# Kernel tuning notes

Measured on AMD Instinct MI355X. Metric: run time of the kernel, lower is better.

## Reference

```python
import jax, jax.numpy as jnp
import numpy as np

DIM = 256
HID = DIM * 16

def setup_inputs() -> dict:
    key = jax.random.key(0)
    ks = jax.random.split(key, 6)
    B, L = 4, 2048
    x = jax.random.normal(ks[0], (B, L, DIM), dtype=jnp.float32)
    # nn.Linear(dim, hidden): weight [H, D], bias [H]
    WB = jax.random.normal(ks[1], (HID, DIM), dtype=jnp.float32) / np.sqrt(DIM)
    bB = jax.random.normal(ks[2], (HID,), dtype=jnp.float32) * 0.01
    # nn.Linear(hidden, dim): weight [D, H], bias [D]
    WC = jax.random.normal(ks[3], (DIM, HID), dtype=jnp.float32) / np.sqrt(HID)
    bC = jax.random.normal(ks[4], (DIM,), dtype=jnp.float32) * 0.01
    A = jax.random.normal(ks[5], (HID,), dtype=jnp.float32)
    return {"x": x, "WB": WB, "bB": bB, "WC": WC, "bC": bC, "A": A}

def reference(x, WB, bB, WC, bC, A):
    # b = B(x): [B, L, H]
    b = jnp.einsum('bld,hd->blh', x, WB) + bB
    a = jax.nn.sigmoid(A)  # [H], time-invariant decay
    # h_t = a * h_{t-1} + b_t  (h_0 from zero state) -> associative scan over L
    a_seq = jnp.broadcast_to(a, b.shape)
    def comb(c1, c2):
        a1, u1 = c1
        a2, u2 = c2
        return (a1 * a2, a2 * u1 + u2)
    _, h = jax.lax.associative_scan(comb, (a_seq, b), axis=1)  # [B, L, H]
    # C(h): [B, L, D]
    return jnp.einsum('blh,dh->bld', h, WC) + bC
```

## Files before the change

kernel.cpp:

```cpp
#include <hip/hip_runtime.h>
#include <hip/hip_bf16.h>

#define DIMSZ 256
#define HID 4096
#define BATCH 4
#define SEQ 2048
#define NCH 64
#define CLEN 32
#define SPLITK2 4
#define KCHUNK (HID / SPLITK2)
#define BM2 64

typedef __bf16 bf16_t;
typedef __bf16 bf16x8 __attribute__((ext_vector_type(8)));
typedef float  f32x4  __attribute__((ext_vector_type(4)));

__device__ __forceinline__ float sigmoidf_dev(float x) {
    return 1.0f / (1.0f + __expf(-x));
}

__device__ __forceinline__ void load_lds16(const bf16_t* g, bf16_t* l) {
    __builtin_amdgcn_global_load_lds(
        (const __attribute__((address_space(1))) void*)g,
        (__attribute__((address_space(3))) void*)l,
        16, 0, 0);
}

__device__ __forceinline__ bf16x8 cvt8(const float* p) {
    bf16x8 o;
    #pragma unroll
    for (int j = 0; j < 8; j++) o[j] = (bf16_t)p[j];
    return o;
}

__global__ void prep_kernel(const float* __restrict__ x,
                            const float* __restrict__ WB,
                            const float* __restrict__ WC,
                            bf16_t* __restrict__ xt,
                            bf16_t* __restrict__ WBt,
                            bf16_t* __restrict__ Wt) {
    int i = blockIdx.x * blockDim.x + threadIdx.x;
    if (i < 262144) {
        int lane = i & 63, m16 = (i >> 6) & 511, ks = i >> 15;
        int row = m16 * 16 + (lane & 15);
        int k   = ks * 32 + (lane >> 4) * 8;
        *(bf16x8*)&xt[(size_t)i * 8] = cvt8(&x[(size_t)row * DIMSZ + k]);
    } else if (i < 393216) {
        int j = i - 262144;
        int lane = j & 63, n16 = (j >> 6) & 255, ks = j >> 14;
        int row = n16 * 16 + (lane & 15);
        int k   = ks * 32 + (lane >> 4) * 8;
        *(bf16x8*)&WBt[(size_t)j * 8] = cvt8(&WB[(size_t)row * DIMSZ + k]);
    } else {
        int j = i - 393216;
        int lane = j & 63, g = (j >> 6) & 15, ks = j >> 10;
        int row = g * 16 + (lane & 15);
        int k   = ks * 32 + (lane >> 4) * 8;
        *(bf16x8*)&Wt[(size_t)j * 8] = cvt8(&WC[(size_t)row * HID + k]);
    }
}

__global__ __launch_bounds__(256)
void gemm1_fused(const bf16_t* __restrict__ xt, const bf16_t* __restrict__ WBt,
                 const float* __restrict__ bias, const float* __restrict__ Adecay,
                 bf16_t* __restrict__ Cg, float* __restrict__ totals)
{
    constexpr int N = HID;
    constexpr int LDTILE = 136;
    __shared__ bf16_t tile[128 * LDTILE];

    const int tid = threadIdx.x, wave = tid >> 6, lane = tid & 63;
    const int wm = wave >> 1, wn = wave & 1, q = lane >> 4, r16 = lane & 15;
    const int mBase = blockIdx.x * 128, nBase = blockIdx.y * 128;
    const int m16Base = blockIdx.x * 8 + wm * 4;
    const int n16Base = blockIdx.y * 8 + wn * 4;

    f32x4 acc[4][4] = {};

    #pragma unroll 2
    for (int ks = 0; ks < 8; ks++) {
        bf16x8 af[4], bfr[4];
        #pragma unroll
        for (int mt = 0; mt < 4; mt++)
            af[mt] = *(const bf16x8*)&xt[(((size_t)ks * 512 + m16Base + mt) * 64 + lane) * 8];
        #pragma unroll
        for (int nt = 0; nt < 4; nt++)
            bfr[nt] = *(const bf16x8*)&WBt[(((size_t)ks * 256 + n16Base + nt) * 64 + lane) * 8];
        #pragma unroll
        for (int mt = 0; mt < 4; mt++)
            #pragma unroll
            for (int nt = 0; nt < 4; nt++)
                acc[mt][nt] = __builtin_amdgcn_mfma_f32_16x16x32_bf16(
                    af[mt], bfr[nt], acc[mt][nt], 0, 0, 0);
    }

    #pragma unroll
    for (int nt = 0; nt < 4; nt++) {
        const int chl = wn * 64 + nt * 16 + r16;
        const float bv = bias[nBase + chl];
        #pragma unroll
        for (int mt = 0; mt < 4; mt++) {
            const int t0 = wm * 64 + mt * 16 + q * 4;
            #pragma unroll
            for (int rg = 0; rg < 4; rg++)
                tile[(t0 + rg) * LDTILE + chl] = (bf16_t)(acc[mt][nt][rg] + bv);
        }
    }
    __syncthreads();

    #pragma unroll
    for (int p = 0; p < 8; p++) {
        const int t = p * 16 + (tid >> 4);
        const int ch8 = (tid & 15) << 3;
        *(bf16x8*)&Cg[(size_t)(mBase + t) * N + nBase + ch8] =
            *(const bf16x8*)&tile[t * LDTILE + ch8];
    }

    #pragma unroll
    for (int t = 0; t < 2; t++) {
        int task = tid + t * 256;
        int ch = task & 127, ck = task >> 7;
        float a = sigmoidf_dev(Adecay[nBase + ch]);
        float tot = 0.f;
        #pragma unroll 8
        for (int i = 0; i < CLEN; i++)
            tot = a * tot + (float)tile[(ck * CLEN + i) * LDTILE + ch];
        int batch = mBase >> 11;
        int cg = ((mBase & 2047) >> 5) + ck;
        totals[(size_t)(batch * NCH + cg) * HID + nBase + ch] = tot;
    }
}

__global__ void scan_carries_kernel(const float* __restrict__ totals,
                                    const float* __restrict__ Adecay,
                                    float* __restrict__ carries)
{
    int gid = blockIdx.x * 64 + threadIdx.x;
    int ch    = gid & (HID - 1);
    int batch = gid >> 12;
    float a = sigmoidf_dev(Adecay[ch]);
    float aC = a;
    #pragma unroll
    for (int i = 0; i < 5; i++) aC *= aC;
    float carry = 0.f;
    #pragma unroll 8
    for (int c = 0; c < NCH; c++) {
        size_t idx = (size_t)(batch * NCH + c) * HID + ch;
        carries[idx] = carry;
        carry = aC * carry + totals[idx];
    }
}

__global__ __launch_bounds__(256)
void gemm2_fused(const bf16_t* __restrict__ bv, const bf16_t* __restrict__ Wt,
                 const float* __restrict__ Adecay, const float* __restrict__ carries,
                 const float* __restrict__ totals, float* __restrict__ P)
{
    constexpr int N = DIMSZ;
    constexpr int CKSTRIDE = BM2 * 32 + 32;
    __shared__ bf16_t hs[8 * CKSTRIDE];

    const int tid = threadIdx.x, wave = tid >> 6, lane = tid & 63;
    const int q = lane >> 4, r16 = lane & 15;
    const int mBase = blockIdx.x * BM2;
    const int kBase = blockIdx.y * KCHUNK;
    const int batch = mBase >> 11;
    const int chunk0 = (mBase & 2047) >> 5;

    f32x4 acc[4][4] = {};

    for (int s = 0; s < KCHUNK / 256; s++) {
        const int chSlab = kBase + s * 256;

        if (s > 0) __syncthreads();

        #pragma unroll
        for (int i = 0; i < 8; i++) {
            int ck = wave * 2 + (i >> 2);
            int g  = i & 3;
            load_lds16(&bv[(size_t)(mBase + g * 16 + (lane >> 2)) * HID
                           + chSlab + ck * 32 + ((lane & 3) << 3)],
                       &hs[ck * CKSTRIDE + g * 512]);
        }

        const int ck = tid >> 5, ch = tid & 31;
        const int c = chSlab + ck * 32 + ch;
        const float a = sigmoidf_dev(Adecay[c]);
        float aC = a;
        #pragma unroll
        for (int i = 0; i < 5; i++) aC *= aC;
        const size_t seedIdx = (size_t)(batch * NCH + chunk0) * HID + c;
        const float carry0 = carries[seedIdx];
        const float carry1 = aC * carry0 + totals[seedIdx];

        __syncthreads();

        {
            bf16_t* hp = &hs[ck * CKSTRIDE + ch];
            float st0 = carry0, st1 = carry1;
            #pragma unroll 8
            for (int t = 0; t < 32; t++) {
                st0 = a * st0 + (float)hp[t * 32];
                st1 = a * st1 + (float)hp[(t + 32) * 32];
                hp[t * 32]        = (bf16_t)st0;
                hp[(t + 32) * 32] = (bf16_t)st1;
            }
        }
        __syncthreads();

        const int ksBase = (kBase >> 5) + s * 8;
        #pragma unroll 2
        for (int cki = 0; cki < 8; cki++) {
            bf16x8 af[4], bfr[4];
            #pragma unroll
            for (int nt = 0; nt < 4; nt++)
                bfr[nt] = *(const bf16x8*)&Wt[
                    (((size_t)(ksBase + cki) * 16 + wave * 4 + nt) * 64 + lane) * 8];
            #pragma unroll
            for (int mt = 0; mt < 4; mt++)
                af[mt] = *(const bf16x8*)&hs[cki * CKSTRIDE + (mt * 16 + r16) * 32 + q * 8];
            #pragma unroll
            for (int mt = 0; mt < 4; mt++)
                #pragma unroll
                for (int nt = 0; nt < 4; nt++)
                    acc[mt][nt] = __builtin_amdgcn_mfma_f32_16x16x32_bf16(
                        af[mt], bfr[nt], acc[mt][nt], 0, 0, 0);
        }
    }

    float* Pb = P + (size_t)blockIdx.y * (BATCH * SEQ) * N;
    #pragma unroll
    for (int nt = 0; nt < 4; nt++) {
        const int col = wave * 64 + nt * 16 + r16;
        #pragma unroll
        for (int mt = 0; mt < 4; mt++) {
            const int row0 = mBase + mt * 16 + q * 4;
            #pragma unroll
            for (int rg = 0; rg < 4; rg++)
                Pb[(size_t)(row0 + rg) * N + col] = acc[mt][nt][rg];
        }
    }
}

__global__ void reduce_out_kernel(const float* __restrict__ P,
                                  const float* __restrict__ bias,
                                  float* __restrict__ out, int MN4) {
    int i = blockIdx.x * blockDim.x + threadIdx.x;
    if (i >= MN4) return;
    int n4 = i & (DIMSZ / 4 - 1);
    float4 acc = ((const float4*)bias)[n4];
    #pragma unroll
    for (int s = 0; s < SPLITK2; s++) {
        float4 p = ((const float4*)P)[(size_t)s * MN4 + i];
        acc.x += p.x; acc.y += p.y; acc.z += p.z; acc.w += p.w;
    }
    ((float4*)out)[i] = acc;
}

extern "C" void kernel_launch(void* const* d_in, const int* in_sizes, int n_in,
                              void* d_out, int out_size, void* d_ws, size_t ws_size,
                              hipStream_t stream)
{
    const float* x  = (const float*)d_in[0];
    const float* WB = (const float*)d_in[1];
    const float* bB = (const float*)d_in[2];
    const float* WC = (const float*)d_in[3];
    const float* bC = (const float*)d_in[4];
    const float* A  = (const float*)d_in[5];

    char* ws = (char*)d_ws;
    size_t off = 0;
    bf16_t* xt   = (bf16_t*)(ws + off); off += (size_t)BATCH * SEQ * DIMSZ * 2;
    bf16_t* WBt  = (bf16_t*)(ws + off); off += (size_t)HID * DIMSZ * 2;
    bf16_t* Wt   = (bf16_t*)(ws + off); off += (size_t)DIMSZ * HID * 2;
    bf16_t* bbuf = (bf16_t*)(ws + off); off += (size_t)BATCH * SEQ * HID * 2;
    float* partials = (float*)(ws + off); off += (size_t)SPLITK2 * BATCH * SEQ * DIMSZ * 4;
    float* totals   = (float*)(ws + off); off += (size_t)BATCH * NCH * HID * 4;
    float* carries  = (float*)(ws + off); off += (size_t)BATCH * NCH * HID * 4;

    const int M = BATCH * SEQ;

    prep_kernel<<<2048, 256, 0, stream>>>(x, WB, WC, xt, WBt, Wt);

    dim3 g1(M / 128, HID / 128);
    gemm1_fused<<<g1, 256, 0, stream>>>(xt, WBt, bB, A, bbuf, totals);

    scan_carries_kernel<<<256, 64, 0, stream>>>(totals, A, carries);

    dim3 g2(M / BM2, SPLITK2);
    gemm2_fused<<<g2, 256, 0, stream>>>(bbuf, Wt, A, carries, totals, partials);
    reduce_out_kernel<<<(M * DIMSZ / 4 + 255) / 256, 256, 0, stream>>>(
        partials, bC, (float*)d_out, M * DIMSZ / 4);
}
```

Before: 152.8 us.

## Fuse split-K reduction into gemm2 via last-block atomic counter

Drops the separate reduce_out kernel. Each gemm2 block bumps a per-row-tile atomic counter after writing its partials, and the last of the SPLITK2 blocks for that tile sums the partials with the bias and writes the output. This saves one kernel launch and lets the reduction overlap with other blocks' GEMM work. In exchange it adds a counter-reset kernel, threadfences and a serialized tail in the last block of each tile.

```diff
diff --git a/kernel.cpp b/kernel.cpp
--- a/kernel.cpp
+++ b/kernel.cpp
@@ -60,6 +60,11 @@
     }
 }
 
+__global__ void init_counters_kernel(int* __restrict__ counters, int n) {
+    int i = blockIdx.x * blockDim.x + threadIdx.x;
+    if (i < n) counters[i] = 0;
+}
+
 __global__ __launch_bounds__(256)
 void gemm1_fused(const bf16_t* __restrict__ xt, const bf16_t* __restrict__ WBt,
                  const float* __restrict__ bias, const float* __restrict__ Adecay,
@@ -154,11 +159,14 @@
 __global__ __launch_bounds__(256)
 void gemm2_fused(const bf16_t* __restrict__ bv, const bf16_t* __restrict__ Wt,
                  const float* __restrict__ Adecay, const float* __restrict__ carries,
-                 const float* __restrict__ totals, float* __restrict__ P)
+                 const float* __restrict__ totals, float* __restrict__ P,
+                 const float* __restrict__ bias, float* __restrict__ outp,
+                 int* __restrict__ counters)
 {
     constexpr int N = DIMSZ;
     constexpr int CKSTRIDE = BM2 * 32 + 32;
     __shared__ bf16_t hs[8 * CKSTRIDE];
+    __shared__ int lastFlag;
 
     const int tid = threadIdx.x, wave = tid >> 6, lane = tid & 63;
     const int q = lane >> 4, r16 = lane & 15;
@@ -240,21 +248,30 @@
                 Pb[(size_t)(row0 + rg) * N + col] = acc[mt][nt][rg];
         }
     }
-}
-
-__global__ void reduce_out_kernel(const float* __restrict__ P,
-                                  const float* __restrict__ bias,
-                                  float* __restrict__ out, int MN4) {
-    int i = blockIdx.x * blockDim.x + threadIdx.x;
-    if (i >= MN4) return;
-    int n4 = i & (DIMSZ / 4 - 1);
-    float4 acc = ((const float4*)bias)[n4];
-    #pragma unroll
-    for (int s = 0; s < SPLITK2; s++) {
-        float4 p = ((const float4*)P)[(size_t)s * MN4 + i];
-        acc.x += p.x; acc.y += p.y; acc.z += p.z; acc.w += p.w;
-    }
-    ((float4*)out)[i] = acc;
+
+    __threadfence();
+    if (tid == 0)
+        lastFlag = (atomicAdd(&counters[blockIdx.x], 1) == SPLITK2 - 1);
+    __syncthreads();
+    if (lastFlag) {
+        __threadfence();
+        const float4* b4 = (const float4*)bias;
+        const float4* P4 = (const float4*)P;
+        float4* o4 = (float4*)outp;
+        constexpr int NW = DIMSZ / 4;
+        #pragma unroll 4
+        for (int i = tid; i < BM2 * NW; i += 256) {
+            int r = i >> 6, c4 = i & 63;
+            size_t rowOff = (size_t)(mBase + r) * NW + c4;
+            float4 v = b4[c4];
+            #pragma unroll
+            for (int sp = 0; sp < SPLITK2; sp++) {
+                float4 p = P4[(size_t)sp * (BATCH * SEQ) * NW + rowOff];
+                v.x += p.x; v.y += p.y; v.z += p.z; v.w += p.w;
+            }
+            o4[rowOff] = v;
+        }
+    }
 }
 
 extern "C" void kernel_launch(void* const* d_in, const int* in_sizes, int n_in,
@@ -277,10 +294,12 @@
     float* partials = (float*)(ws + off); off += (size_t)SPLITK2 * BATCH * SEQ * DIMSZ * 4;
     float* totals   = (float*)(ws + off); off += (size_t)BATCH * NCH * HID * 4;
     float* carries  = (float*)(ws + off); off += (size_t)BATCH * NCH * HID * 4;
+    int* counters   = (int*)(ws + off);  off += 128 * sizeof(int);
 
     const int M = BATCH * SEQ;
 
     prep_kernel<<<2048, 256, 0, stream>>>(x, WB, WC, xt, WBt, Wt);
+    init_counters_kernel<<<1, 128, 0, stream>>>(counters, 128);
 
     dim3 g1(M / 128, HID / 128);
     gemm1_fused<<<g1, 256, 0, stream>>>(xt, WBt, bB, A, bbuf, totals);
@@ -288,7 +307,6 @@
     scan_carries_kernel<<<256, 64, 0, stream>>>(totals, A, carries);
 
     dim3 g2(M / BM2, SPLITK2);
-    gemm2_fused<<<g2, 256, 0, stream>>>(bbuf, Wt, A, carries, totals, partials);
-    reduce_out_kernel<<<(M * DIMSZ / 4 + 255) / 256, 256, 0, stream>>>(
-        partials, bC, (float*)d_out, M * DIMSZ / 4);
-}
+    gemm2_fused<<<g2, 256, 0, stream>>>(bbuf, Wt, A, carries, totals, partials,
+                                        bC, (float*)d_out, counters);
+}
```

New measurement: 232.6 us. +52.2%, slower.
